# Kernel optimization log

Measured on AMD Instinct MI355X. Metric: run time of the kernel, lower is better.

## Reference

```python
import jax, jax.numpy as jnp
import numpy as np

B, S, D, H = 4, 2048, 1024, 16
HD = D // H  # head dim = 64


def setup_inputs() -> dict:
    key = jax.random.key(0)
    k1, k2, k3 = jax.random.split(key, 3)
    scale = 1.0 / np.sqrt(D).astype(np.float32)
    x = jax.random.normal(k1, (B, S, D), dtype=jnp.float32)
    # q/k slices of nn.MultiheadAttention's in_proj (v and out_proj never
    # influence the returned values since x_t is discarded by forward)
    wq = jax.random.normal(k2, (D, D), dtype=jnp.float32) * scale
    wk = jax.random.normal(k3, (D, D), dtype=jnp.float32) * scale
    bq = jnp.zeros((D,), dtype=jnp.float32)
    bk = jnp.zeros((D,), dtype=jnp.float32)
    # 8 contiguous scale blocks of 256 tokens; last boundary == S
    scales_idx = (jnp.arange(1, 9, dtype=jnp.int64) * (S // 8))
    return {"x": x, "wq": wq, "wk": wk, "bq": bq, "bk": bk,
            "scales_idx": scales_idx}


def reference(x, wq, wk, bq, bk, scales_idx):
    b, s, d = x.shape
    # project q, k and split heads: [B, H, S, HD]
    q = (x @ wq.T + bq).reshape(b, s, H, HD).transpose(0, 2, 1, 3)
    k = (x @ wk.T + bk).reshape(b, s, H, HD).transpose(0, 2, 1, 3)
    inv_sqrt_hd = jnp.asarray(1.0 / np.sqrt(HD), dtype=x.dtype)
    scores = jnp.einsum('bhqd,bhkd->bhqk', q, k) * inv_sqrt_hd  # [B,H,S,S]
    # block-diagonal mask: token i belongs to the block whose right boundary
    # is the first scales_idx entry strictly greater than i
    pos = jnp.arange(s)
    seg = jnp.searchsorted(scales_idx, pos, side='right')  # [S]
    allowed = seg[:, None] == seg[None, :]                  # [S,S] bool
    scores = jnp.where(allowed[None, None], scores, -jnp.inf)
    w = jax.nn.softmax(scores, axis=-1)  # every row has >=1 allowed entry
    weights_attn = jnp.mean(w, axis=1)   # average over heads -> [B,S,S]
    return (x, weights_attn)
```

## Files before the change

kernel.cpp:

```cpp
#include <hip/hip_runtime.h>
#include <hip/hip_bf16.h>
#include <math.h>

#define BB 4
#define SS 2048
#define DD 1024
#define HH 16
#define HD 64
#define MM (BB*SS)
#define NN (2*DD)

typedef __attribute__((ext_vector_type(8))) short short8;
typedef __attribute__((ext_vector_type(4))) float f32x4;
typedef unsigned short ushort_t;

__device__ __forceinline__ void gload16(const void* g, void* l) {
    __builtin_amdgcn_global_load_lds((const __attribute__((address_space(1))) unsigned int*)g,
                                     (__attribute__((address_space(3))) unsigned int*)l,
                                     16, 0, 0);
}

__global__ __launch_bounds__(256)
void copy_cast(const float* __restrict__ x, float* __restrict__ out_x,
               __hip_bfloat16* __restrict__ xb, int n8)
{
    int i = blockIdx.x * 256 + threadIdx.x;
    if (i >= n8) return;
    const float4* s = (const float4*)x + (size_t)i * 2;
    float4 a = s[0], b = s[1];
    float4* o = (float4*)out_x + (size_t)i * 2;
    o[0] = a; o[1] = b;
    __hip_bfloat16 tmp[8];
    tmp[0] = __float2bfloat16(a.x); tmp[1] = __float2bfloat16(a.y);
    tmp[2] = __float2bfloat16(a.z); tmp[3] = __float2bfloat16(a.w);
    tmp[4] = __float2bfloat16(b.x); tmp[5] = __float2bfloat16(b.y);
    tmp[6] = __float2bfloat16(b.z); tmp[7] = __float2bfloat16(b.w);
    *(float4*)&xb[(size_t)i * 8] = *(float4*)tmp;
}

__global__ __launch_bounds__(256)
void cast_w(const float* __restrict__ wq, const float* __restrict__ wk,
            __hip_bfloat16* __restrict__ wb)
{
    const int half = (DD * DD) / 8;
    int i = blockIdx.x * 256 + threadIdx.x;
    if (i >= 2 * half) return;
    const float* src = (i < half) ? wq : wk;
    int j = (i < half) ? i : i - half;
    const float4* s = (const float4*)src + (size_t)j * 2;
    float4 a = s[0], b = s[1];
    __hip_bfloat16 tmp[8];
    tmp[0] = __float2bfloat16(a.x); tmp[1] = __float2bfloat16(a.y);
    tmp[2] = __float2bfloat16(a.z); tmp[3] = __float2bfloat16(a.w);
    tmp[4] = __float2bfloat16(b.x); tmp[5] = __float2bfloat16(b.y);
    tmp[6] = __float2bfloat16(b.z); tmp[7] = __float2bfloat16(b.w);
    *(float4*)&wb[(size_t)i * 8] = *(float4*)tmp;
}

__global__ __launch_bounds__(256, 2)
void proj_mfma(const ushort_t* __restrict__ xb, const ushort_t* __restrict__ wb,
               const float* __restrict__ bq, const float* __restrict__ bk,
               __hip_bfloat16* __restrict__ Qb, __hip_bfloat16* __restrict__ Kb)
{
    __shared__ __align__(16) ushort_t As[128 * 64];
    __shared__ __align__(16) ushort_t Bs[128 * 64];

    const int t = threadIdx.x;
    const int wv = t >> 6, lane = t & 63, quad = lane >> 4, l15 = lane & 15;
    const int m0 = blockIdx.x * 128, n0 = blockIdx.y * 128;
    const int wm = (wv & 1) * 64, wn = (wv >> 1) * 64;

    f32x4 acc[4][4];
    #pragma unroll
    for (int mt = 0; mt < 4; ++mt)
        #pragma unroll
        for (int nt = 0; nt < 4; ++nt) acc[mt][nt] = (f32x4){0.f, 0.f, 0.f, 0.f};

    for (int kt = 0; kt < DD; kt += 64) {
        __syncthreads();
        #pragma unroll
        for (int call = 0; call < 4; ++call) {
            int c = call * 256 + t;
            int row = c >> 3, ch = c & 7;
            int gch = ch ^ (row & 7);
            gload16(xb + (size_t)(m0 + row) * DD + kt + gch * 8,
                    As + ((size_t)call * 256 + wv * 64) * 8);
            gload16(wb + (size_t)(n0 + row) * DD + kt + gch * 8,
                    Bs + ((size_t)call * 256 + wv * 64) * 8);
        }
        __syncthreads();
        #pragma unroll
        for (int ks = 0; ks < 2; ++ks) {
            short8 a[4], bb_[4];
            #pragma unroll
            for (int mt = 0; mt < 4; ++mt) {
                int r = wm + mt * 16 + l15;
                int sl = r * 8 + ((ks * 4 + quad) ^ (r & 7));
                a[mt] = *(const short8*)&As[sl * 8];
            }
            #pragma unroll
            for (int nt = 0; nt < 4; ++nt) {
                int r = wn + nt * 16 + l15;
                int sl = r * 8 + ((ks * 4 + quad) ^ (r & 7));
                bb_[nt] = *(const short8*)&Bs[sl * 8];
            }
            #pragma unroll
            for (int mt = 0; mt < 4; ++mt)
                #pragma unroll
                for (int nt = 0; nt < 4; ++nt)
                    acc[mt][nt] = __builtin_amdgcn_mfma_f32_16x16x32_bf16(
                        a[mt], bb_[nt], acc[mt][nt], 0, 0, 0);
        }
    }

    const bool isQ = (n0 < DD);
    const float* bias = isQ ? bq : bk;
    __hip_bfloat16* outp = isQ ? Qb : Kb;
    const int nc0 = isQ ? n0 : (n0 - DD);
    #pragma unroll
    for (int nt = 0; nt < 4; ++nt) {
        const int nc = nc0 + wn + nt * 16 + l15;
        const float bv = bias[nc];
        #pragma unroll
        for (int mt = 0; mt < 4; ++mt)
            #pragma unroll
            for (int reg = 0; reg < 4; ++reg) {
                int m = m0 + wm + mt * 16 + quad * 4 + reg;
                outp[(size_t)m * DD + nc] = __float2bfloat16(acc[mt][nt][reg] + bv);
            }
    }
}

__global__ __launch_bounds__(256, 1)
void attn_block(const ushort_t* __restrict__ Qb, const ushort_t* __restrict__ Kb,
                const int* __restrict__ scales, float* __restrict__ outw)
{
    __shared__ __align__(16) char smem[73728];
    ushort_t* KsB = (ushort_t*)smem;
    ushort_t* QsB = (ushort_t*)(smem + 65536);
    float (*comb)[256] = (float(*)[256])smem;

    const int bid = blockIdx.x;
    const int rt = bid & 7, blk = (bid >> 3) & 7, bb = bid >> 6;
    const int start = blk ? scales[blk - 1] : 0;

    const int t = threadIdx.x;
    const int wv = t >> 6, lane = t & 63, quad = lane >> 4, l15 = lane & 15;
    const int rg = wv & 1, hg = wv >> 1;

    f32x4 accm[16];
    #pragma unroll
    for (int nt = 0; nt < 16; ++nt) accm[nt] = (f32x4){0.f, 0.f, 0.f, 0.f};

    const int qrow0 = start + rt * 32;

    for (int i = 0; i < 8; ++i) {
        __syncthreads();
        #pragma unroll
        for (int half = 0; half < 2; ++half) {
            const int h = half * 8 + i;
            ushort_t* Kl = KsB + half * (256 * 64);
            ushort_t* Ql = QsB + half * (32 * 64);
            #pragma unroll
            for (int round = 0; round < 8; ++round) {
                int c = round * 256 + t;
                int row = c >> 3, ch = c & 7;
                int gch = ch ^ (row & 7);
                gload16(Kb + (size_t)(bb * SS + start + row) * DD + h * HD + gch * 8,
                        Kl + ((size_t)round * 256 + wv * 64) * 8);
            }
            {
                int row = t >> 3, ch = t & 7;
                int gch = ch ^ (row & 7);
                gload16(Qb + (size_t)(bb * SS + qrow0 + row) * DD + h * HD + gch * 8,
                        Ql + ((size_t)wv * 64) * 8);
            }
        }
        __syncthreads();

        const ushort_t* Ks = KsB + hg * (256 * 64);
        const ushort_t* Qs = QsB + hg * (32 * 64);

        short8 af[2];
        #pragma unroll
        for (int ks = 0; ks < 2; ++ks) {
            int qr = rg * 16 + l15;
            int sl = qr * 8 + ((ks * 4 + quad) ^ (qr & 7));
            af[ks] = *(const short8*)&Qs[sl * 8];
        }
        f32x4 sc[16];
        #pragma unroll
        for (int nt = 0; nt < 16; ++nt) {
            sc[nt] = (f32x4){0.f, 0.f, 0.f, 0.f};
            #pragma unroll
            for (int ks = 0; ks < 2; ++ks) {
                int kr = nt * 16 + l15;
                int sl = kr * 8 + ((ks * 4 + quad) ^ (kr & 7));
                short8 bf = *(const short8*)&Ks[sl * 8];
                sc[nt] = __builtin_amdgcn_mfma_f32_16x16x32_bf16(af[ks], bf, sc[nt], 0, 0, 0);
            }
        }
        float rs[4] = {0.f, 0.f, 0.f, 0.f};
        #pragma unroll
        for (int nt = 0; nt < 16; ++nt) {
            #pragma unroll
            for (int r = 0; r < 4; ++r) {
                float p = __expf(sc[nt][r] * 0.125f);
                sc[nt][r] = p;
                rs[r] += p;
            }
        }
        #pragma unroll
        for (int r = 0; r < 4; ++r) {
            #pragma unroll
            for (int off = 1; off < 16; off <<= 1) rs[r] += __shfl_xor(rs[r], off, 64);
            rs[r] = 1.0f / rs[r];
        }
        #pragma unroll
        for (int nt = 0; nt < 16; ++nt)
            #pragma unroll
            for (int r = 0; r < 4; ++r) accm[nt][r] += sc[nt][r] * rs[r];
    }

    __syncthreads();
    if (hg == 0) {
        #pragma unroll
        for (int nt = 0; nt < 16; ++nt)
            #pragma unroll
            for (int r = 0; r < 4; ++r)
                comb[rg * 16 + quad * 4 + r][nt * 16 + l15] = accm[nt][r];
    }
    __syncthreads();
    if (hg == 1) {
        #pragma unroll
        for (int nt = 0; nt < 16; ++nt)
            #pragma unroll
            for (int r = 0; r < 4; ++r)
                comb[rg * 16 + quad * 4 + r][nt * 16 + l15] += accm[nt][r];
    }
    __syncthreads();

    const float s16 = 1.0f / (float)HH;
    const size_t orow0 = (size_t)bb * SS + qrow0;
    #pragma unroll
    for (int it = 0; it < 64; ++it) {
        int flat = it * 256 + t;
        int row = flat >> 9;
        int col = (flat & 511) * 4;
        float4 v = make_float4(0.f, 0.f, 0.f, 0.f);
        unsigned lc = (unsigned)(col - start);
        if (lc < 256u) {
            const float* c = &comb[row][lc];
            v = make_float4(c[0] * s16, c[1] * s16, c[2] * s16, c[3] * s16);
        }
        *(float4*)&outw[(orow0 + row) * SS + col] = v;
    }
}

extern "C" void kernel_launch(void* const* d_in, const int* in_sizes, int n_in,
                              void* d_out, int out_size, void* d_ws, size_t ws_size,
                              hipStream_t stream)
{
    const float* x  = (const float*)d_in[0];
    const float* wq = (const float*)d_in[1];
    const float* wk = (const float*)d_in[2];
    const float* bq = (const float*)d_in[3];
    const float* bk = (const float*)d_in[4];
    const int* scales = (const int*)d_in[5];

    float* out_x = (float*)d_out;
    float* out_w = out_x + (size_t)BB * SS * DD;

    char* w = (char*)d_ws;
    __hip_bfloat16* xb = (__hip_bfloat16*)(w);
    __hip_bfloat16* wb = (__hip_bfloat16*)(w + 16777216);
    __hip_bfloat16* Qb = (__hip_bfloat16*)(w + 20971520);
    __hip_bfloat16* Kb = (__hip_bfloat16*)(w + 37748736);

    copy_cast<<<4096, 256, 0, stream>>>(x, out_x, xb, (MM * DD) / 8);
    cast_w<<<1024, 256, 0, stream>>>(wq, wk, wb);

    dim3 pgrid(MM / 128, NN / 128);
    proj_mfma<<<pgrid, 256, 0, stream>>>((const ushort_t*)xb, (const ushort_t*)wb,
                                         bq, bk, Qb, Kb);

    attn_block<<<256, 256, 0, stream>>>((const ushort_t*)Qb, (const ushort_t*)Kb,
                                        scales, out_w);
}
```

Measured before the change: 213.6 us.

## Load Q/K fragments directly from global into registers, drop LDS staging

Replaces the LDS-staged attention kernel with one where each wave handles 4 heads for a 16-row query tile and loads Q/K MFMA operands straight from global memory into registers. Grid doubles to 512 blocks with an XCD-aware block mapping, and launch bounds allow 2 blocks per CU. This removes the per-head barriers and LDS staging traffic and raises occupancy. In exchange, K loads are uncoalesced 16-byte reads repeated across blocks and depend on L2 hits, and the cross-wave reduction now needs more serialized barrier steps.

```diff
diff --git a/kernel.cpp b/kernel.cpp
--- a/kernel.cpp
+++ b/kernel.cpp
@@ -131,75 +131,49 @@
     }
 }
 
-__global__ __launch_bounds__(256, 1)
-void attn_block(const ushort_t* __restrict__ Qb, const ushort_t* __restrict__ Kb,
-                const int* __restrict__ scales, float* __restrict__ outw)
-{
-    __shared__ __align__(16) char smem[73728];
-    ushort_t* KsB = (ushort_t*)smem;
-    ushort_t* QsB = (ushort_t*)(smem + 65536);
-    float (*comb)[256] = (float(*)[256])smem;
-
-    const int bid = blockIdx.x;
-    const int rt = bid & 7, blk = (bid >> 3) & 7, bb = bid >> 6;
+__global__ __launch_bounds__(256, 2)
+void attn_reg(const ushort_t* __restrict__ Qb, const ushort_t* __restrict__ Kb,
+              const int* __restrict__ scales, float* __restrict__ outw)
+{
+    __shared__ float comb[16][256];
+
+    const int gid = blockIdx.x;
+    const int xcd = gid & 7, slot = gid >> 3;
+    const int rt = slot & 15;
+    const int group = ((slot >> 4) << 3) | xcd;
+    const int bb = group >> 3, blk = group & 7;
     const int start = blk ? scales[blk - 1] : 0;
 
     const int t = threadIdx.x;
     const int wv = t >> 6, lane = t & 63, quad = lane >> 4, l15 = lane & 15;
-    const int rg = wv & 1, hg = wv >> 1;
+
+    const int qrow0 = start + rt * 16;
+    const ushort_t* Qrow = Qb + ((size_t)(bb * SS + qrow0 + l15)) * DD;
+    const ushort_t* Kbase = Kb + ((size_t)(bb * SS + start + l15)) * DD;
 
     f32x4 accm[16];
     #pragma unroll
     for (int nt = 0; nt < 16; ++nt) accm[nt] = (f32x4){0.f, 0.f, 0.f, 0.f};
 
-    const int qrow0 = start + rt * 32;
-
-    for (int i = 0; i < 8; ++i) {
-        __syncthreads();
-        #pragma unroll
-        for (int half = 0; half < 2; ++half) {
-            const int h = half * 8 + i;
-            ushort_t* Kl = KsB + half * (256 * 64);
-            ushort_t* Ql = QsB + half * (32 * 64);
-            #pragma unroll
-            for (int round = 0; round < 8; ++round) {
-                int c = round * 256 + t;
-                int row = c >> 3, ch = c & 7;
-                int gch = ch ^ (row & 7);
-                gload16(Kb + (size_t)(bb * SS + start + row) * DD + h * HD + gch * 8,
-                        Kl + ((size_t)round * 256 + wv * 64) * 8);
-            }
-            {
-                int row = t >> 3, ch = t & 7;
-                int gch = ch ^ (row & 7);
-                gload16(Qb + (size_t)(bb * SS + qrow0 + row) * DD + h * HD + gch * 8,
-                        Ql + ((size_t)wv * 64) * 8);
-            }
-        }
-        __syncthreads();
-
-        const ushort_t* Ks = KsB + hg * (256 * 64);
-        const ushort_t* Qs = QsB + hg * (32 * 64);
-
-        short8 af[2];
-        #pragma unroll
-        for (int ks = 0; ks < 2; ++ks) {
-            int qr = rg * 16 + l15;
-            int sl = qr * 8 + ((ks * 4 + quad) ^ (qr & 7));
-            af[ks] = *(const short8*)&Qs[sl * 8];
-        }
+    for (int hh = 0; hh < 4; ++hh) {
+        const int h = wv * 4 + hh;
+        const int ho = h * HD + quad * 8;
+
+        short8 af0 = *(const short8*)(Qrow + ho);
+        short8 af1 = *(const short8*)(Qrow + ho + 32);
+
         f32x4 sc[16];
         #pragma unroll
         for (int nt = 0; nt < 16; ++nt) {
-            sc[nt] = (f32x4){0.f, 0.f, 0.f, 0.f};
-            #pragma unroll
-            for (int ks = 0; ks < 2; ++ks) {
-                int kr = nt * 16 + l15;
-                int sl = kr * 8 + ((ks * 4 + quad) ^ (kr & 7));
-                short8 bf = *(const short8*)&Ks[sl * 8];
-                sc[nt] = __builtin_amdgcn_mfma_f32_16x16x32_bf16(af[ks], bf, sc[nt], 0, 0, 0);
-            }
-        }
+            const ushort_t* kp = Kbase + (size_t)(nt * 16) * DD + ho;
+            short8 b0 = *(const short8*)(kp);
+            short8 b1 = *(const short8*)(kp + 32);
+            f32x4 s = (f32x4){0.f, 0.f, 0.f, 0.f};
+            s = __builtin_amdgcn_mfma_f32_16x16x32_bf16(af0, b0, s, 0, 0, 0);
+            s = __builtin_amdgcn_mfma_f32_16x16x32_bf16(af1, b1, s, 0, 0, 0);
+            sc[nt] = s;
+        }
+
         float rs[4] = {0.f, 0.f, 0.f, 0.f};
         #pragma unroll
         for (int nt = 0; nt < 16; ++nt) {
@@ -222,28 +196,30 @@
             for (int r = 0; r < 4; ++r) accm[nt][r] += sc[nt][r] * rs[r];
     }
 
+    if (wv == 0) {
+        #pragma unroll
+        for (int nt = 0; nt < 16; ++nt)
+            #pragma unroll
+            for (int r = 0; r < 4; ++r)
+                comb[quad * 4 + r][nt * 16 + l15] = accm[nt][r];
+    }
     __syncthreads();
-    if (hg == 0) {
-        #pragma unroll
-        for (int nt = 0; nt < 16; ++nt)
-            #pragma unroll
-            for (int r = 0; r < 4; ++r)
-                comb[rg * 16 + quad * 4 + r][nt * 16 + l15] = accm[nt][r];
-    }
-    __syncthreads();
-    if (hg == 1) {
-        #pragma unroll
-        for (int nt = 0; nt < 16; ++nt)
-            #pragma unroll
-            for (int r = 0; r < 4; ++r)
-                comb[rg * 16 + quad * 4 + r][nt * 16 + l15] += accm[nt][r];
-    }
-    __syncthreads();
+    #pragma unroll
+    for (int w = 1; w < 4; ++w) {
+        if (wv == w) {
+            #pragma unroll
+            for (int nt = 0; nt < 16; ++nt)
+                #pragma unroll
+                for (int r = 0; r < 4; ++r)
+                    comb[quad * 4 + r][nt * 16 + l15] += accm[nt][r];
+        }
+        __syncthreads();
+    }
 
     const float s16 = 1.0f / (float)HH;
     const size_t orow0 = (size_t)bb * SS + qrow0;
     #pragma unroll
-    for (int it = 0; it < 64; ++it) {
+    for (int it = 0; it < 32; ++it) {
         int flat = it * 256 + t;
         int row = flat >> 9;
         int col = (flat & 511) * 4;
@@ -284,6 +260,6 @@
     proj_mfma<<<pgrid, 256, 0, stream>>>((const ushort_t*)xb, (const ushort_t*)wb,
                                          bq, bk, Qb, Kb);
 
-    attn_block<<<256, 256, 0, stream>>>((const ushort_t*)Qb, (const ushort_t*)Kb,
-                                        scales, out_w);
-}
+    attn_reg<<<512, 256, 0, stream>>>((const ushort_t*)Qb, (const ushort_t*)Kb,
+                                      scales, out_w);
+}
```

New measurement: 221.2 us. 1.04x slower.
